# Performance work log

Measured on AMD Instinct MI355X. Metric: run time of the kernel, lower is better.

Reference implementation:

```python
import jax, jax.numpy as jnp
import numpy as np

H = 8          # num heads
LN_EPS = 1e-5  # torch LayerNorm default

_SHAPES = {
    'src': (1024, 8, 256), 'pos': (1024, 8, 256), 'query_embed': (80, 8, 256), 'cam_mask': (8, 80, 1024),
    'enc_qkv_w': (2, 768, 256), 'enc_qkv_b': (2, 768), 'enc_out_w': (2, 256, 256), 'enc_out_b': (2, 256),
    'enc_ln1_g': (2, 256), 'enc_ln1_b': (2, 256),
    'enc_ff1_w': (2, 2048, 256), 'enc_ff1_b': (2, 2048), 'enc_ff2_w': (2, 256, 2048), 'enc_ff2_b': (2, 256),
    'enc_ln2_g': (2, 256), 'enc_ln2_b': (2, 256),
    'dec_sa_qkv_w': (2, 768, 256), 'dec_sa_qkv_b': (2, 768), 'dec_sa_out_w': (2, 256, 256), 'dec_sa_out_b': (2, 256),
    'dec_ln1_g': (2, 256), 'dec_ln1_b': (2, 256),
    'dec_ca_qkv_w': (2, 768, 256), 'dec_ca_qkv_b': (2, 768), 'dec_ca_out_w': (2, 256, 256), 'dec_ca_out_b': (2, 256),
    'dec_ln2_g': (2, 256), 'dec_ln2_b': (2, 256),
    'dec_ff1_w': (2, 2048, 256), 'dec_ff1_b': (2, 2048), 'dec_ff2_w': (2, 256, 2048), 'dec_ff2_b': (2, 256),
    'dec_ln3_g': (2, 256), 'dec_ln3_b': (2, 256),
    'dec_norm_g': (256,), 'dec_norm_b': (256,),
}


def setup_inputs() -> dict:
    key = jax.random.key(0)
    out = {}
    for i, (name, sh) in enumerate(_SHAPES.items()):
        k = jax.random.fold_in(key, i)
        if name.endswith('_g'):
            out[name] = jnp.ones(sh, jnp.float32)
        elif name.endswith('ln1_b') or name.endswith('ln2_b') or name.endswith('ln3_b') or name == 'dec_norm_b':
            out[name] = jnp.zeros(sh, jnp.float32)
        else:
            scale = 1.0 if name in ('src', 'pos', 'query_embed', 'cam_mask') else 0.02
            out[name] = jax.random.normal(k, sh, dtype=jnp.float32) * scale
    return out


def layer_norm(x, g, b):
    mu = jnp.mean(x, axis=-1, keepdims=True)
    var = jnp.mean(jnp.square(x - mu), axis=-1, keepdims=True)
    return (x - mu) * jax.lax.rsqrt(var + LN_EPS) * g + b


def mha(q_in, k_in, v_in, qkv_w, qkv_b, out_w, out_b, bias=None):
    # q_in: [L,B,D], k_in/v_in: [S,B,D]; torch layout: projections are x @ W.T + b
    L, B, D = q_in.shape
    S = k_in.shape[0]
    hd = D // H
    wq, wk, wv = qkv_w[:D], qkv_w[D:2 * D], qkv_w[2 * D:]
    bq, bk, bv = qkv_b[:D], qkv_b[D:2 * D], qkv_b[2 * D:]
    q = (q_in @ wq.T + bq).reshape(L, B, H, hd).transpose(1, 2, 0, 3)  # [B,H,L,hd]
    k = (k_in @ wk.T + bk).reshape(S, B, H, hd).transpose(1, 2, 0, 3)  # [B,H,S,hd]
    v = (v_in @ wv.T + bv).reshape(S, B, H, hd).transpose(1, 2, 0, 3)
    logits = jnp.einsum('bhld,bhsd->bhls', q, k) * (1.0 / np.sqrt(hd))
    if bias is not None:
        logits = logits + bias[:, None, :, :]  # CAM bias broadcast over heads
    attn = jax.nn.softmax(logits, axis=-1)
    o = jnp.einsum('bhls,bhsd->bhld', attn, v).transpose(2, 0, 1, 3).reshape(L, B, D)
    return o @ out_w.T + out_b


def reference(src, pos, query_embed, cam_mask,
              enc_qkv_w, enc_qkv_b, enc_out_w, enc_out_b, enc_ln1_g, enc_ln1_b,
              enc_ff1_w, enc_ff1_b, enc_ff2_w, enc_ff2_b, enc_ln2_g, enc_ln2_b,
              dec_sa_qkv_w, dec_sa_qkv_b, dec_sa_out_w, dec_sa_out_b, dec_ln1_g, dec_ln1_b,
              dec_ca_qkv_w, dec_ca_qkv_b, dec_ca_out_w, dec_ca_out_b, dec_ln2_g, dec_ln2_b,
              dec_ff1_w, dec_ff1_b, dec_ff2_w, dec_ff2_b, dec_ln3_g, dec_ln3_b,
              dec_norm_g, dec_norm_b):
    n_enc = enc_qkv_w.shape[0]
    n_dec = dec_sa_qkv_w.shape[0]
    # --- encoder (post-norm DETR style, pos added to q,k) ---
    mem = src
    for i in range(n_enc):
        qk = mem + pos
        a = mha(qk, qk, mem, enc_qkv_w[i], enc_qkv_b[i], enc_out_w[i], enc_out_b[i])
        mem = layer_norm(mem + a, enc_ln1_g[i], enc_ln1_b[i])
        f = jax.nn.relu(mem @ enc_ff1_w[i].T + enc_ff1_b[i]) @ enc_ff2_w[i].T + enc_ff2_b[i]
        mem = layer_norm(mem + f, enc_ln2_g[i], enc_ln2_b[i])
    # --- decoder: tgt starts at zeros (Q2L), query_embed is query_pos ---
    tgt = jnp.zeros_like(query_embed)
    for i in range(n_dec):
        qk = tgt + query_embed
        sa = mha(qk, qk, tgt, dec_sa_qkv_w[i], dec_sa_qkv_b[i], dec_sa_out_w[i], dec_sa_out_b[i])
        tgt = layer_norm(tgt + sa, dec_ln1_g[i], dec_ln1_b[i])
        ca = mha(tgt + query_embed, mem + pos, mem,
                 dec_ca_qkv_w[i], dec_ca_qkv_b[i], dec_ca_out_w[i], dec_ca_out_b[i],
                 bias=cam_mask)  # MA: CAM-derived additive attention bias [B,L,S]
        tgt = layer_norm(tgt + ca, dec_ln2_g[i], dec_ln2_b[i])
        f = jax.nn.relu(tgt @ dec_ff1_w[i].T + dec_ff1_b[i]) @ dec_ff2_w[i].T + dec_ff2_b[i]
        tgt = layer_norm(tgt + f, dec_ln3_g[i], dec_ln3_b[i])
    out = layer_norm(tgt, dec_norm_g, dec_norm_b)
    return out[None]  # [1, L, B, D] as in TransformerDecoder's output.unsqueeze(0)
```

## Files before the change

kernel.cpp:

```cpp
#include <hip/hip_runtime.h>
#include <hip/hip_bf16.h>
#include <cstdint>
#include <cstddef>

typedef __hip_bfloat16 bf16;
typedef float f4 __attribute__((ext_vector_type(4)));
typedef float f32x4 __attribute__((ext_vector_type(4)));
typedef short s8v __attribute__((ext_vector_type(8)));
typedef unsigned short u16x4 __attribute__((ext_vector_type(4)));
typedef unsigned short u16x8 __attribute__((ext_vector_type(8)));

#define LN_EPS 1e-5f
#define LOG2E 1.4426950408889634f

#if __has_builtin(__builtin_amdgcn_exp2f)
__device__ __forceinline__ float EXP2(float x) { return __builtin_amdgcn_exp2f(x); }
#else
__device__ __forceinline__ float EXP2(float x) {
  float r; asm("v_exp_f32 %0, %1" : "=v"(r) : "v"(x)); return r;
}
#endif

__device__ __forceinline__ void async_cp16(const void* g, void* lds) {
  __builtin_amdgcn_global_load_lds(
      (const __attribute__((address_space(1))) unsigned int*)g,
      (__attribute__((address_space(3))) unsigned int*)lds, 16, 0, 0);
}

__device__ __forceinline__ uint32_t pkbf(float lo, float hi) {
#if __has_builtin(__builtin_amdgcn_perm)
  uint32_t l = __builtin_bit_cast(uint32_t, lo) + 0x8000u;
  uint32_t h = __builtin_bit_cast(uint32_t, hi) + 0x8000u;
  return __builtin_amdgcn_perm(h, l, 0x07060302u);
#else
  uint32_t l = __builtin_bit_cast(uint32_t, lo) + 0x8000u;
  uint32_t h = __builtin_bit_cast(uint32_t, hi) + 0x8000u;
  return (l >> 16) | (h & 0xFFFF0000u);
#endif
}

#define NCAST 16
struct CastArgs {
  const float* in[NCAST];
  bf16* out[NCAST];
  int end4[NCAST];
  int nseg;
};

__global__ __launch_bounds__(256) void cast_multi(CastArgs a, int total4) {
  int i = blockIdx.x * 256 + threadIdx.x;
  if (i >= total4) return;
  int s = 0;
  while (i >= a.end4[s]) ++s;
  int j = i - (s ? a.end4[s - 1] : 0);
  f4 v = ((const f4*)a.in[s])[j];
  u16x4 o;
#pragma unroll
  for (int c = 0; c < 4; ++c) {
    bf16 h = __float2bfloat16(v[c]);
    o[c] = *reinterpret_cast<unsigned short*>(&h);
  }
  ((u16x4*)a.out[s])[j] = o;
}

__global__ __launch_bounds__(256) void scale_f32_kernel(const float* __restrict__ in,
                                                        float* __restrict__ out,
                                                        float s, int n4) {
  int i = blockIdx.x * 256 + threadIdx.x;
  if (i < n4) {
    f4 v = ((const f4*)in)[i];
    ((f4*)out)[i] = v * s;
  }
}

__global__ __launch_bounds__(256) void add_bf16_kernel(const float* __restrict__ a,
                                                       const float* __restrict__ b,
                                                       bf16* __restrict__ out, int n4) {
  int i = blockIdx.x * 256 + threadIdx.x;
  if (i < n4) {
    f4 x = ((const f4*)a)[i];
    f4 y = ((const f4*)b)[i];
    u16x4 o;
#pragma unroll
    for (int j = 0; j < 4; ++j) {
      bf16 h = __float2bfloat16(x[j] + y[j]);
      o[j] = *reinterpret_cast<unsigned short*>(&h);
    }
    ((u16x4*)out)[i] = o;
  }
}

template <int TB, int MODE, int SPLITK>
__global__ __launch_bounds__(256, 2) void mfma_gemm(
    const bf16* __restrict__ A, const bf16* __restrict__ W,
    const float* __restrict__ bias, float* __restrict__ C,
    bf16* __restrict__ Cb, int M, int N, int K, int HL, float qscale) {
  constexpr int WM = TB / 2, WN = TB / 2;
  constexpr int MR = WM / 16, NR = WN / 16;
  constexpr int NCH = TB / 32;
  __shared__ __attribute__((aligned(16))) unsigned short SH[TB * 128];
  unsigned short (*As)[64] = (unsigned short(*)[64])SH;
  unsigned short (*Ws)[64] = (unsigned short(*)[64])(SH + TB * 64);
  const int tid = threadIdx.x;
  const int lane = tid & 63, wave = tid >> 6;
  const int wr = wave >> 1, wc = wave & 1;
  const int bm = blockIdx.x * TB, bn = blockIdx.y * TB;
  const int fr = lane & 15, fo = lane >> 4;
  const int srowi = lane >> 3;
  const int slot = lane & 7;
  const int gcol = (slot ^ srowi) * 8;

  const int kchunk = K / SPLITK;
  const int kbeg = (SPLITK > 1) ? blockIdx.z * kchunk : 0;

  f32x4 acc[MR][NR] = {};

  for (int k0 = kbeg; k0 < kbeg + kchunk; k0 += 64) {
    __syncthreads();
#pragma unroll
    for (int c = 0; c < NCH; ++c) {
      int rbase = wave * (TB / 4) + c * 8;
      int row = rbase + srowi;
      async_cp16(A + (size_t)(bm + row) * K + k0 + gcol, &As[rbase][0]);
      async_cp16(W + (size_t)(bn + row) * K + k0 + gcol, &Ws[rbase][0]);
    }
    __syncthreads();
#pragma unroll
    for (int ks = 0; ks < 2; ++ks) {
      s8v a[MR], b[NR];
#pragma unroll
      for (int mi = 0; mi < MR; ++mi) {
        int row = wr * WM + mi * 16 + fr;
        a[mi] = *(const s8v*)((const char*)&As[0][0] + row * 128 +
                              ((ks * 64 + fo * 16) ^ ((row & 7) << 4)));
      }
#pragma unroll
      for (int ni = 0; ni < NR; ++ni) {
        int row = wc * WN + ni * 16 + fr;
        b[ni] = *(const s8v*)((const char*)&Ws[0][0] + row * 128 +
                              ((ks * 64 + fo * 16) ^ ((row & 7) << 4)));
      }
#pragma unroll
      for (int mi = 0; mi < MR; ++mi)
#pragma unroll
        for (int ni = 0; ni < NR; ++ni)
          acc[mi][ni] = __builtin_amdgcn_mfma_f32_16x16x32_bf16(
              a[mi], b[ni], acc[mi][ni], 0, 0, 0);
    }
  }

  const int r0 = (lane >> 4) * 4;

  if (MODE == 5) {
    __syncthreads();
    unsigned short (*T)[72] = (unsigned short(*)[72])SH;
#pragma unroll
    for (int mi = 0; mi < MR; ++mi)
#pragma unroll
      for (int ni = 0; ni < NR; ++ni) {
        int colL = wc * WN + ni * 16 + fr;
        float bv = bias[bn + colL];
#pragma unroll
        for (int r = 0; r < 4; ++r) {
          int rowL = wr * WM + mi * 16 + r0 + r;
          bf16 hv = __float2bfloat16(acc[mi][ni][r] + bv);
          T[colL][rowL] = *(unsigned short*)&hv;
        }
      }
    __syncthreads();
    const int lbase = bm >> 3;
#pragma unroll
    for (int jj = 0; jj < 2; ++jj) {
      int cid = tid * 2 + jj;
      int colL = cid >> 3, bb = cid & 7;
      int c = bn + colL;
      int sec = c >> 8, hh = (c >> 5) & 7, d = c & 31;
      u16x8 v;
#pragma unroll
      for (int l = 0; l < 8; ++l) v[l] = T[colL][bb + 8 * l];
      *(u16x8*)(Cb + (size_t)sec * ((size_t)64 * 32 * HL) +
                ((size_t)(bb * 8 + hh) * 32 + d) * HL + lbase) = v;
    }
    return;
  }

  float* Cz = (MODE == 4) ? C + (size_t)blockIdx.z * M * N : C;
#pragma unroll
  for (int mi = 0; mi < MR; ++mi) {
#pragma unroll
    for (int ni = 0; ni < NR; ++ni) {
      int col = bn + wc * WN + ni * 16 + fr;
      float bv = (MODE == 4) ? 0.f : bias[col];
#pragma unroll
      for (int r = 0; r < 4; ++r) {
        int row = bm + wr * WM + mi * 16 + r0 + r;
        float t = acc[mi][ni][r] + bv;
        if (MODE == 2) t = fmaxf(t, 0.f);
        if (MODE == 0) {
          C[(size_t)row * N + col] = t;
        } else if (MODE == 4) {
          Cz[(size_t)row * N + col] = t;
        } else if (MODE == 3) {
          int l = row >> 3, bb = row & 7;
          int sec = col >> 8, hh = (col >> 5) & 7, d = col & 31;
          if (sec == 0) t *= qscale;
          Cb[(size_t)sec * ((size_t)64 * HL * 32) +
             ((size_t)(bb * 8 + hh) * HL + l) * 32 + d] = __float2bfloat16(t);
        } else {
          Cb[(size_t)row * N + col] = __float2bfloat16(t);
        }
      }
    }
  }
}

template <int HAS_BIAS, int PARTIAL, int NW>
__global__ __launch_bounds__(NW * 64, 3) void attn_mfma(
    const bf16* __restrict__ Qh, const bf16* __restrict__ Kh,
    const bf16* __restrict__ VhT, const float* __restrict__ bias,
    bf16* __restrict__ O, float* __restrict__ PO, float* __restrict__ PM,
    float* __restrict__ PL, int L, int S, int SC) {
  __shared__ __attribute__((aligned(16))) uint32_t Ps2[NW][16][68];
  const int tid = threadIdx.x;
  const int lane = tid & 63, wave = tid >> 6;
  const int fr = lane & 15, fo = lane >> 4;
  const int bh = blockIdx.x;
  const int b = bh >> 3, h = bh & 7;
  const int q0 = blockIdx.y * (NW * 16) + wave * 16;
  const int q = q0 + fr;

  const int cz = PARTIAL ? blockIdx.z : 0;
  const int sb = PARTIAL ? cz * SC : 0;
  const int se = PARTIAL ? min(S, sb + SC) : S;

  s8v qf = {};
  if (q < L) qf = *(const s8v*)(Qh + ((size_t)bh * L + q) * 32 + fo * 8);

  const float* brow = nullptr;
  if (HAS_BIAS) brow = bias + ((size_t)b * L + (q < L ? q : L - 1)) * S;

  float m = -1e30f, lsum = 0.f;
  f32x4 oacc[2] = {};

  for (int s0 = sb; s0 < se; s0 += 128) {
    s8v kf[8];
#pragma unroll
    for (int i = 0; i < 8; ++i) {
      int key = s0 + (i >> 2) * 64 + (i & 3) * 16 + fr;
      kf[i] = *(const s8v*)(Kh + ((size_t)bh * S + key) * 32 + fo * 8);
    }
    s8v vf[2][4];
#pragma unroll
    for (int dh = 0; dh < 2; ++dh)
#pragma unroll
      for (int ks = 0; ks < 4; ++ks)
        vf[dh][ks] = *(const s8v*)(VhT + ((size_t)bh * 32 + dh * 16 + fr) * S +
                                   s0 + ks * 32 + fo * 8);

    float lg[32];
#pragma unroll
    for (int i = 0; i < 8; ++i) {
      f32x4 z = {};
      f32x4 sa = __builtin_amdgcn_mfma_f32_16x16x32_bf16(kf[i], qf, z, 0, 0, 0);
#pragma unroll
      for (int r = 0; r < 4; ++r) lg[i * 4 + r] = sa[r];
    }

    if (HAS_BIAS) {
#pragma unroll
      for (int i = 0; i < 8; ++i) {
        f4 bv = *(const f4*)(brow + s0 + (i >> 2) * 64 + (i & 3) * 16 + 4 * fo);
#pragma unroll
        for (int r = 0; r < 4; ++r) lg[i * 4 + r] += bv[r];
      }
    }

    if (s0 + 128 > se) {
#pragma unroll
      for (int i = 0; i < 8; ++i)
#pragma unroll
        for (int r = 0; r < 4; ++r) {
          int key = s0 + (i >> 2) * 64 + (i & 3) * 16 + 4 * fo + r;
          if (key >= se) lg[i * 4 + r] = -1e30f;
        }
    }

    float t[8];
#pragma unroll
    for (int i = 0; i < 8; ++i)
      t[i] = fmaxf(fmaxf(lg[i * 4], lg[i * 4 + 1]),
                   fmaxf(lg[i * 4 + 2], lg[i * 4 + 3]));
    float u0 = fmaxf(fmaxf(t[0], t[1]), fmaxf(t[2], t[3]));
    float u1 = fmaxf(fmaxf(t[4], t[5]), fmaxf(t[6], t[7]));
    float tm = fmaxf(u0, u1);
    tm = fmaxf(tm, __shfl_xor(tm, 16));
    tm = fmaxf(tm, __shfl_xor(tm, 32));

    if (__any(tm > m + 8.f)) {
      float nm = fmaxf(m, tm);
      float rs = EXP2(m - nm);
      m = nm;
      lsum *= rs;
#pragma unroll
      for (int r = 0; r < 4; ++r) { oacc[0][r] *= rs; oacc[1][r] *= rs; }
    }

    float ps = 0.f;
#pragma unroll
    for (int i = 0; i < 32; ++i) {
      lg[i] = EXP2(lg[i] - m);
      ps += lg[i];
    }
    lsum += ps;

#pragma unroll
    for (int i = 0; i < 8; ++i) {
      uint32_t w0 = pkbf(lg[i * 4 + 0], lg[i * 4 + 1]);
      uint32_t w1 = pkbf(lg[i * 4 + 2], lg[i * 4 + 3]);
      uint64_t w = (uint64_t)w0 | ((uint64_t)w1 << 32);
      *(uint64_t*)&Ps2[wave][fr][(i >> 2) * 32 + (i & 3) * 8 + 2 * fo] = w;
    }

    s8v pf[4];
#pragma unroll
    for (int ks = 0; ks < 4; ++ks)
      pf[ks] = *(const s8v*)&Ps2[wave][fr][ks * 16 + 4 * fo];

#pragma unroll
    for (int dh = 0; dh < 2; ++dh)
#pragma unroll
      for (int ks = 0; ks < 4; ++ks)
        oacc[dh] = __builtin_amdgcn_mfma_f32_16x16x32_bf16(
            vf[dh][ks], pf[ks], oacc[dh], 0, 0, 0);
  }

  lsum += __shfl_xor(lsum, 16);
  lsum += __shfl_xor(lsum, 32);

  if (q < L) {
    if (PARTIAL) {
      size_t pi = ((size_t)cz * 64 + bh) * L + q;
      float* po = PO + pi * 32;
#pragma unroll
      for (int dh = 0; dh < 2; ++dh) {
        f4 t2;
#pragma unroll
        for (int r = 0; r < 4; ++r) t2[r] = oacc[dh][r];
        *(f4*)(po + dh * 16 + 4 * fo) = t2;
      }
      if (fo == 0) { PM[pi] = m; PL[pi] = lsum; }
    } else {
      float inv = 1.f / lsum;
      bf16* op = O + ((size_t)q * 8 + b) * 256 + h * 32;
#pragma unroll
      for (int dh = 0; dh < 2; ++dh) {
        uint32_t w0 = pkbf(oacc[dh][0] * inv, oacc[dh][1] * inv);
        uint32_t w1 = pkbf(oacc[dh][2] * inv, oacc[dh][3] * inv);
        *(uint32_t*)(op + dh * 16 + 4 * fo) = w0;
        *(uint32_t*)(op + dh * 16 + 4 * fo + 2) = w1;
      }
    }
  }
}

__global__ __launch_bounds__(256) void attn_combine(
    const float* __restrict__ PO, const float* __restrict__ PM,
    const float* __restrict__ PL, bf16* __restrict__ O, int L, int NC) {
  int gid = blockIdx.x * 256 + threadIdx.x;
  if (gid >= 64 * L * 32) return;
  int d = gid & 31;
  int rem = gid >> 5;
  int q = rem % L, bh = rem / L;
  int b = bh >> 3, h = bh & 7;
  float M = -1e30f;
  for (int c = 0; c < NC; ++c) M = fmaxf(M, PM[((size_t)c * 64 + bh) * L + q]);
  float lsum = 0.f, o = 0.f;
  for (int c = 0; c < NC; ++c) {
    size_t pi = ((size_t)c * 64 + bh) * L + q;
    float w = EXP2(PM[pi] - M);
    lsum += PL[pi] * w;
    o += PO[pi * 32 + d] * w;
  }
  O[((size_t)q * 8 + b) * 256 + h * 32 + d] = __float2bfloat16(o / lsum);
}

__global__ __launch_bounds__(256) void ln_kernel(
    const float* __restrict__ x, const float* __restrict__ res,
    const float* __restrict__ parts, int nparts, int pstride,
    const float* __restrict__ gbias,
    const float* __restrict__ g, const float* __restrict__ b,
    float* __restrict__ out, bf16* __restrict__ outb) {
  const int row = blockIdx.x, tid = threadIdx.x;
  size_t idx = (size_t)row * 256 + tid;
  float v = x[idx];
  if (res) v += res[idx];
  if (parts) {
    for (int z = 0; z < nparts; ++z) v += parts[(size_t)z * pstride + idx];
  }
  if (gbias) v += gbias[tid];
  float s = v, s2 = v * v;
#pragma unroll
  for (int off = 32; off >= 1; off >>= 1) {
    s += __shfl_down(s, off);
    s2 += __shfl_down(s2, off);
  }
  __shared__ float red[8];
  int wv = tid >> 6;
  if ((tid & 63) == 0) { red[wv] = s; red[4 + wv] = s2; }
  __syncthreads();
  if (tid == 0) {
    float ts = red[0] + red[1] + red[2] + red[3];
    float ts2 = red[4] + red[5] + red[6] + red[7];
    float mu = ts * (1.f / 256.f);
    float var = ts2 * (1.f / 256.f) - mu * mu;
    red[0] = mu;
    red[1] = rsqrtf(var + LN_EPS);
  }
  __syncthreads();
  float y = (v - red[0]) * red[1] * g[tid] + b[tid];
  if (out) out[idx] = y;
  if (outb) outb[idx] = __float2bfloat16(y);
}

extern "C" void kernel_launch(void* const* d_in, const int* in_sizes, int n_in,
                              void* d_out, int out_size, void* d_ws, size_t ws_size,
                              hipStream_t stream) {
  const float* src         = (const float*)d_in[0];
  const float* pos         = (const float*)d_in[1];
  const float* query_embed = (const float*)d_in[2];
  const float* cam_mask    = (const float*)d_in[3];
  const float* enc_qkv_w   = (const float*)d_in[4];
  const float* enc_qkv_b   = (const float*)d_in[5];
  const float* enc_out_w   = (const float*)d_in[6];
  const float* enc_out_b   = (const float*)d_in[7];
  const float* enc_ln1_g   = (const float*)d_in[8];
  const float* enc_ln1_b   = (const float*)d_in[9];
  const float* enc_ff1_w   = (const float*)d_in[10];
  const float* enc_ff1_b   = (const float*)d_in[11];
  const float* enc_ff2_w   = (const float*)d_in[12];
  const float* enc_ff2_b   = (const float*)d_in[13];
  const float* enc_ln2_g   = (const float*)d_in[14];
  const float* enc_ln2_b   = (const float*)d_in[15];
  const float* dec_sa_qkv_w= (const float*)d_in[16];
  const float* dec_sa_qkv_b= (const float*)d_in[17];
  const float* dec_sa_out_w= (const float*)d_in[18];
  const float* dec_sa_out_b= (const float*)d_in[19];
  const float* dec_ln1_g   = (const float*)d_in[20];
  const float* dec_ln1_b   = (const float*)d_in[21];
  const float* dec_ca_qkv_w= (const float*)d_in[22];
  const float* dec_ca_qkv_b= (const float*)d_in[23];
  const float* dec_ca_out_w= (const float*)d_in[24];
  const float* dec_ca_out_b= (const float*)d_in[25];
  const float* dec_ln2_g   = (const float*)d_in[26];
  const float* dec_ln2_b   = (const float*)d_in[27];
  const float* dec_ff1_w   = (const float*)d_in[28];
  const float* dec_ff1_b   = (const float*)d_in[29];
  const float* dec_ff2_w   = (const float*)d_in[30];
  const float* dec_ff2_b   = (const float*)d_in[31];
  const float* dec_ln3_g   = (const float*)d_in[32];
  const float* dec_ln3_b   = (const float*)d_in[33];
  const float* dec_norm_g  = (const float*)d_in[34];
  const float* dec_norm_b  = (const float*)d_in[35];

  size_t off = 0;
  char* base = (char*)d_ws;
  auto af = [&](size_t n) { float* p = (float*)(base + off); off += n * 4; return p; };
  auto ab = [&](size_t n) { bf16*  p = (bf16*)(base + off);  off += n * 2; return p; };

  float* mem  = af(2097152);
  float* r1   = af(2097152);
  float* PO   = af(8388608);
  float* pm   = af(262144);
  float* pl   = af(262144);
  float* cmlog= af(655360);
  float* pb   = af(1024);
  float* tgt  = af(163840);
  float* tpr  = af(163840);
  bf16* memb  = ab(2097152);
  bf16* qkb   = ab(2097152);
  bf16* aob   = ab(2097152);
  bf16* ffb   = ab(16777216);
  bf16* bufQ  = ab(4194304);
  bf16* bufK  = ab(4194304);
  bf16* bufV  = ab(4194304);
  bf16* bufVsa= ab(172032);
  bf16* tgtb  = ab(163840);
  bf16* tqkb  = ab(163840);
  bf16* taob  = ab(163840);
  bf16* tffb  = ab(1310720);
  bf16* w_enc_qkv = ab(393216);
  bf16* w_enc_out = ab(131072);
  bf16* w_enc_ff1 = ab(1048576);
  bf16* w_enc_ff2 = ab(1048576);
  bf16* w_sa_qkv  = ab(393216);
  bf16* w_sa_out  = ab(131072);
  bf16* w_ca_q    = ab(131072);
  bf16* w_ca_kv   = ab(262144);
  bf16* w_ca_out  = ab(131072);
  bf16* w_dec_ff1 = ab(1048576);
  bf16* w_dec_ff2 = ab(1048576);

  const float qscale = 0.17677669529663687f * LOG2E;

  {
    CastArgs ca;
    const float* ins[NCAST] = {
        enc_qkv_w, enc_out_w, enc_ff1_w, enc_ff2_w,
        dec_sa_qkv_w, dec_sa_out_w,
        dec_ca_qkv_w,
        dec_ca_qkv_w + 65536,
        dec_ca_qkv_w + 131072,
        dec_ca_qkv_w + 196608,
        dec_ca_qkv_w + 262144,
        dec_ca_qkv_w + 327680,
        dec_ca_out_w, dec_ff1_w, dec_ff2_w, src};
    bf16* outs[NCAST] = {
        w_enc_qkv, w_enc_out, w_enc_ff1, w_enc_ff2,
        w_sa_qkv, w_sa_out,
        w_ca_q,
        w_ca_kv,
        w_ca_kv + 131072,
        w_ca_q + 65536,
        w_ca_kv + 65536,
        w_ca_kv + 196608,
        w_ca_out, w_dec_ff1, w_dec_ff2, memb};
    int n4s[NCAST] = {98304, 32768, 262144, 262144, 98304, 32768,
                      16384, 16384, 16384, 16384, 16384, 16384,
                      32768, 262144, 262144, 524288};
    int acc = 0;
    for (int s = 0; s < NCAST; ++s) {
      ca.in[s] = ins[s]; ca.out[s] = outs[s];
      acc += n4s[s]; ca.end4[s] = acc;
    }
    ca.nseg = NCAST;
    cast_multi<<<(acc + 255) / 256, 256, 0, stream>>>(ca, acc);
  }
  scale_f32_kernel<<<640, 256, 0, stream>>>(cam_mask, cmlog, LOG2E, 163840);
  hipMemcpyAsync(mem, src, (size_t)2097152 * 4, hipMemcpyDeviceToDevice, stream);
  hipMemcpyAsync(pb,       dec_ca_qkv_b + 256,       1024, hipMemcpyDeviceToDevice, stream);
  hipMemcpyAsync(pb + 256, dec_ca_qkv_b + 768 + 256, 1024, hipMemcpyDeviceToDevice, stream);
  hipMemcpyAsync(pb + 512, dec_ca_qkv_b + 512,       1024, hipMemcpyDeviceToDevice, stream);
  hipMemcpyAsync(pb + 768, dec_ca_qkv_b + 768 + 512, 1024, hipMemcpyDeviceToDevice, stream);

  auto g64_f = [&](const bf16* A, const bf16* W, const float* bias, float* C,
                   int M, int N, int K) {
    mfma_gemm<64, 0, 1><<<dim3(M / 64, N / 64), 256, 0, stream>>>(
        A, W, bias, C, nullptr, M, N, K, 0, 1.f);
  };
  auto g64_head = [&](const bf16* A, const bf16* W, const float* bias, bf16* Cb,
                      int M, int N, int K, int HL, float qs) {
    mfma_gemm<64, 3, 1><<<dim3(M / 64, N / 64), 256, 0, stream>>>(
        A, W, bias, nullptr, Cb, M, N, K, HL, qs);
  };
  auto g64_headT = [&](const bf16* A, const bf16* W, const float* bias, bf16* Cb,
                       int M, int N, int K, int HL) {
    mfma_gemm<64, 5, 1><<<dim3(M / 64, N / 64), 256, 0, stream>>>(
        A, W, bias, nullptr, Cb, M, N, K, HL, 1.f);
  };
  auto g64_relu = [&](const bf16* A, const bf16* W, const float* bias, bf16* Cb,
                      int M, int N, int K) {
    mfma_gemm<64, 2, 1><<<dim3(M / 64, N / 64), 256, 0, stream>>>(
        A, W, bias, nullptr, Cb, M, N, K, 0, 1.f);
  };
  auto g128_relu = [&](const bf16* A, const bf16* W, const float* bias, bf16* Cb,
                       int M, int N, int K) {
    mfma_gemm<128, 2, 1><<<dim3(M / 128, N / 128), 256, 0, stream>>>(
        A, W, bias, nullptr, Cb, M, N, K, 0, 1.f);
  };

  for (int i = 0; i < 2; ++i) {
    const bf16* wq = w_enc_qkv + (size_t)i * 196608;
    const float* qkvb = enc_qkv_b + (size_t)i * 768;
    add_bf16_kernel<<<2048, 256, 0, stream>>>(mem, pos, qkb, 524288);
    g64_head(qkb, wq, qkvb, bufQ, 8192, 512, 256, 1024, qscale);
    g64_headT(memb, wq + 131072, qkvb + 512, bufV, 8192, 256, 256, 1024);
    attn_mfma<0, 0, 4><<<dim3(64, 16), 256, 0, stream>>>(
        bufQ, bufQ + 2097152, bufV, nullptr, aob, nullptr, nullptr, nullptr,
        1024, 1024, 0);
    g64_f(aob, w_enc_out + (size_t)i * 65536, enc_out_b + i * 256, r1,
          8192, 256, 256);
    ln_kernel<<<8192, 256, 0, stream>>>(mem, r1, nullptr, 0, 0, nullptr,
                                        enc_ln1_g + i * 256, enc_ln1_b + i * 256,
                                        mem, memb);
    g128_relu(memb, w_enc_ff1 + (size_t)i * 524288, enc_ff1_b + i * 2048, ffb,
              8192, 2048, 256);
    mfma_gemm<128, 4, 4><<<dim3(64, 2, 4), 256, 0, stream>>>(
        ffb, w_enc_ff2 + (size_t)i * 524288, nullptr, PO, nullptr,
        8192, 256, 2048, 0, 1.f);
    ln_kernel<<<8192, 256, 0, stream>>>(mem, nullptr, PO, 4, 2097152,
                                        enc_ff2_b + i * 256,
                                        enc_ln2_g + i * 256, enc_ln2_b + i * 256,
                                        mem, memb);
  }

  hipMemsetAsync(tgt, 0, (size_t)163840 * 4, stream);
  hipMemsetAsync(tgtb, 0, (size_t)163840 * 2, stream);
  add_bf16_kernel<<<2048, 256, 0, stream>>>(mem, pos, qkb, 524288);

  g64_head(qkb, w_ca_kv, pb, bufK, 8192, 512, 256, 1024, 1.f);
  g64_headT(memb, w_ca_kv + 131072, pb + 512, bufV, 8192, 512, 256, 1024);

  for (int i = 0; i < 2; ++i) {
    const bf16* wsa = w_sa_qkv + (size_t)i * 196608;
    const float* sab = dec_sa_qkv_b + (size_t)i * 768;
    const float* cab = dec_ca_qkv_b + (size_t)i * 768;

    add_bf16_kernel<<<160, 256, 0, stream>>>(tgt, query_embed, tqkb, 40960);
    g64_head(tqkb, wsa, sab, bufQ, 640, 512, 256, 80, qscale);
    g64_headT(tgtb, wsa + 131072, sab + 512, bufVsa, 640, 256, 256, 80);
    attn_mfma<0, 0, 1><<<dim3(64, 5), 64, 0, stream>>>(
        bufQ, bufQ + 163840, bufVsa, nullptr, taob, nullptr, nullptr, nullptr,
        80, 80, 0);
    g64_f(taob, w_sa_out + (size_t)i * 65536, dec_sa_out_b + i * 256, tpr,
          640, 256, 256);
    ln_kernel<<<640, 256, 0, stream>>>(tgt, tpr, nullptr, 0, 0, nullptr,
                                       dec_ln1_g + i * 256, dec_ln1_b + i * 256,
                                       tgt, tgtb);
    add_bf16_kernel<<<160, 256, 0, stream>>>(tgt, query_embed, tqkb, 40960);
    g64_head(tqkb, w_ca_q + (size_t)i * 65536, cab, bufQ, 640, 256, 256, 80, qscale);
    attn_mfma<1, 1, 1><<<dim3(64, 5, 8), 64, 0, stream>>>(
        bufQ, bufK + (size_t)i * 2097152, bufV + (size_t)i * 2097152, cmlog,
        nullptr, PO, pm, pl, 80, 1024, 128);
    attn_combine<<<640, 256, 0, stream>>>(PO, pm, pl, taob, 80, 8);
    g64_f(taob, w_ca_out + (size_t)i * 65536, dec_ca_out_b + i * 256, tpr,
          640, 256, 256);
    ln_kernel<<<640, 256, 0, stream>>>(tgt, tpr, nullptr, 0, 0, nullptr,
                                       dec_ln2_g + i * 256, dec_ln2_b + i * 256,
                                       tgt, tgtb);
    g64_relu(tgtb, w_dec_ff1 + (size_t)i * 524288, dec_ff1_b + i * 2048, tffb,
             640, 2048, 256);
    mfma_gemm<64, 4, 4><<<dim3(10, 4, 4), 256, 0, stream>>>(
        tffb, w_dec_ff2 + (size_t)i * 524288, nullptr, PO, nullptr,
        640, 256, 2048, 0, 1.f);
    ln_kernel<<<640, 256, 0, stream>>>(tgt, nullptr, PO, 4, 163840,
                                       dec_ff2_b + i * 256,
                                       dec_ln3_g + i * 256, dec_ln3_b + i * 256,
                                       tgt, tgtb);
  }

  ln_kernel<<<640, 256, 0, stream>>>(tgt, nullptr, nullptr, 0, 0, nullptr,
                                     dec_norm_g, dec_norm_b,
                                     (float*)d_out, nullptr);
}
```

Baseline: 433.3 us.

## Split attention loop into two independent online-softmax streams per 128-key step

Each 128-key iteration of the attention kernel is split into two 64-key halves, each with its own running max, sum and output accumulator, merged only once at the end. This gives the scheduler two independent dependency chains to interleave, so MFMA, exp and shuffle latency can overlap. The lazy rescale under __any is replaced by an unconditional rescale each step, and bias loads are issued up front with the K/V loads. The cost is more registers for duplicated state, which may hurt occupancy. The loop also appears to assume an even number of 64-key groups in the range, or it reads past its chunk.

```diff
diff --git a/kernel.cpp b/kernel.cpp
--- a/kernel.cpp
+++ b/kernel.cpp
@@ -220,7 +220,7 @@
     const bf16* __restrict__ VhT, const float* __restrict__ bias,
     bf16* __restrict__ O, float* __restrict__ PO, float* __restrict__ PM,
     float* __restrict__ PL, int L, int S, int SC) {
-  __shared__ __attribute__((aligned(16))) uint32_t Ps2[NW][16][68];
+  __shared__ __attribute__((aligned(16))) uint32_t Ps2[NW][2][16][36];
   const int tid = threadIdx.x;
   const int lane = tid & 63, wave = tid >> 6;
   const int fr = lane & 15, fo = lane >> 4;
@@ -232,6 +232,7 @@
   const int cz = PARTIAL ? blockIdx.z : 0;
   const int sb = PARTIAL ? cz * SC : 0;
   const int se = PARTIAL ? min(S, sb + SC) : S;
+  const int ng = (se - sb + 63) >> 6;
 
   s8v qf = {};
   if (q < L) qf = *(const s8v*)(Qh + ((size_t)bh * L + q) * 32 + fo * 8);
@@ -239,100 +240,140 @@
   const float* brow = nullptr;
   if (HAS_BIAS) brow = bias + ((size_t)b * L + (q < L ? q : L - 1)) * S;
 
-  float m = -1e30f, lsum = 0.f;
-  f32x4 oacc[2] = {};
-
-  for (int s0 = sb; s0 < se; s0 += 128) {
-    s8v kf[8];
-#pragma unroll
-    for (int i = 0; i < 8; ++i) {
-      int key = s0 + (i >> 2) * 64 + (i & 3) * 16 + fr;
-      kf[i] = *(const s8v*)(Kh + ((size_t)bh * S + key) * 32 + fo * 8);
-    }
-    s8v vf[2][4];
+  const bf16* Kbase = Kh + (size_t)bh * S * 32;
+  const bf16* Vbase = VhT + (size_t)bh * 32 * S;
+
+  float mA = -1e30f, lsA = 0.f, mB = -1e30f, lsB = 0.f;
+  f32x4 oA[2] = {}, oB[2] = {};
+
+  for (int g = 0; g < ng; g += 2) {
+    const int sA = sb + g * 64, sB = sA + 64;
+
+    s8v kA[4], kB[4], vA[2][2], vB[2][2];
+#pragma unroll
+    for (int kb = 0; kb < 4; ++kb) {
+      kA[kb] = *(const s8v*)(Kbase + (size_t)(sA + kb * 16 + fr) * 32 + fo * 8);
+      kB[kb] = *(const s8v*)(Kbase + (size_t)(sB + kb * 16 + fr) * 32 + fo * 8);
+    }
 #pragma unroll
     for (int dh = 0; dh < 2; ++dh)
 #pragma unroll
-      for (int ks = 0; ks < 4; ++ks)
-        vf[dh][ks] = *(const s8v*)(VhT + ((size_t)bh * 32 + dh * 16 + fr) * S +
-                                   s0 + ks * 32 + fo * 8);
-
-    float lg[32];
-#pragma unroll
-    for (int i = 0; i < 8; ++i) {
+      for (int ks = 0; ks < 2; ++ks) {
+        vA[dh][ks] = *(const s8v*)(Vbase + (size_t)(dh * 16 + fr) * S +
+                                   sA + ks * 32 + fo * 8);
+        vB[dh][ks] = *(const s8v*)(Vbase + (size_t)(dh * 16 + fr) * S +
+                                   sB + ks * 32 + fo * 8);
+      }
+    f4 bA[4], bB[4];
+    if (HAS_BIAS) {
+#pragma unroll
+      for (int kb = 0; kb < 4; ++kb) {
+        bA[kb] = *(const f4*)(brow + sA + kb * 16 + 4 * fo);
+        bB[kb] = *(const f4*)(brow + sB + kb * 16 + 4 * fo);
+      }
+    }
+
+    float lgA[16], lgB[16];
+#pragma unroll
+    for (int kb = 0; kb < 4; ++kb) {
       f32x4 z = {};
-      f32x4 sa = __builtin_amdgcn_mfma_f32_16x16x32_bf16(kf[i], qf, z, 0, 0, 0);
-#pragma unroll
-      for (int r = 0; r < 4; ++r) lg[i * 4 + r] = sa[r];
-    }
-
+      f32x4 sa = __builtin_amdgcn_mfma_f32_16x16x32_bf16(kA[kb], qf, z, 0, 0, 0);
+#pragma unroll
+      for (int r = 0; r < 4; ++r) lgA[kb * 4 + r] = sa[r];
+    }
+#pragma unroll
+    for (int kb = 0; kb < 4; ++kb) {
+      f32x4 z = {};
+      f32x4 sa = __builtin_amdgcn_mfma_f32_16x16x32_bf16(kB[kb], qf, z, 0, 0, 0);
+#pragma unroll
+      for (int r = 0; r < 4; ++r) lgB[kb * 4 + r] = sa[r];
+    }
     if (HAS_BIAS) {
 #pragma unroll
-      for (int i = 0; i < 8; ++i) {
-        f4 bv = *(const f4*)(brow + s0 + (i >> 2) * 64 + (i & 3) * 16 + 4 * fo);
-#pragma unroll
-        for (int r = 0; r < 4; ++r) lg[i * 4 + r] += bv[r];
-      }
-    }
-
-    if (s0 + 128 > se) {
-#pragma unroll
-      for (int i = 0; i < 8; ++i)
-#pragma unroll
-        for (int r = 0; r < 4; ++r) {
-          int key = s0 + (i >> 2) * 64 + (i & 3) * 16 + 4 * fo + r;
-          if (key >= se) lg[i * 4 + r] = -1e30f;
-        }
-    }
-
-    float t[8];
-#pragma unroll
-    for (int i = 0; i < 8; ++i)
-      t[i] = fmaxf(fmaxf(lg[i * 4], lg[i * 4 + 1]),
-                   fmaxf(lg[i * 4 + 2], lg[i * 4 + 3]));
-    float u0 = fmaxf(fmaxf(t[0], t[1]), fmaxf(t[2], t[3]));
-    float u1 = fmaxf(fmaxf(t[4], t[5]), fmaxf(t[6], t[7]));
-    float tm = fmaxf(u0, u1);
-    tm = fmaxf(tm, __shfl_xor(tm, 16));
-    tm = fmaxf(tm, __shfl_xor(tm, 32));
-
-    if (__any(tm > m + 8.f)) {
-      float nm = fmaxf(m, tm);
-      float rs = EXP2(m - nm);
-      m = nm;
-      lsum *= rs;
-#pragma unroll
-      for (int r = 0; r < 4; ++r) { oacc[0][r] *= rs; oacc[1][r] *= rs; }
-    }
-
-    float ps = 0.f;
-#pragma unroll
-    for (int i = 0; i < 32; ++i) {
-      lg[i] = EXP2(lg[i] - m);
-      ps += lg[i];
-    }
-    lsum += ps;
-
-#pragma unroll
-    for (int i = 0; i < 8; ++i) {
-      uint32_t w0 = pkbf(lg[i * 4 + 0], lg[i * 4 + 1]);
-      uint32_t w1 = pkbf(lg[i * 4 + 2], lg[i * 4 + 3]);
-      uint64_t w = (uint64_t)w0 | ((uint64_t)w1 << 32);
-      *(uint64_t*)&Ps2[wave][fr][(i >> 2) * 32 + (i & 3) * 8 + 2 * fo] = w;
-    }
-
-    s8v pf[4];
-#pragma unroll
-    for (int ks = 0; ks < 4; ++ks)
-      pf[ks] = *(const s8v*)&Ps2[wave][fr][ks * 16 + 4 * fo];
-
+      for (int i = 0; i < 16; ++i) { lgA[i] += bA[i >> 2][i & 3]; lgB[i] += bB[i >> 2][i & 3]; }
+    }
+    if (sB + 64 > se) {
+#pragma unroll
+      for (int i = 0; i < 16; ++i) {
+        int keyA = sA + (i >> 2) * 16 + 4 * fo + (i & 3);
+        int keyB = sB + (i >> 2) * 16 + 4 * fo + (i & 3);
+        if (keyA >= se) lgA[i] = -1e30f;
+        if (keyB >= se) lgB[i] = -1e30f;
+      }
+    }
+
+    float tA, tB;
+    {
+      float a0 = fmaxf(fmaxf(lgA[0], lgA[1]), fmaxf(lgA[2], lgA[3]));
+      float a1 = fmaxf(fmaxf(lgA[4], lgA[5]), fmaxf(lgA[6], lgA[7]));
+      float a2 = fmaxf(fmaxf(lgA[8], lgA[9]), fmaxf(lgA[10], lgA[11]));
+      float a3 = fmaxf(fmaxf(lgA[12], lgA[13]), fmaxf(lgA[14], lgA[15]));
+      tA = fmaxf(fmaxf(a0, a1), fmaxf(a2, a3));
+      float b0 = fmaxf(fmaxf(lgB[0], lgB[1]), fmaxf(lgB[2], lgB[3]));
+      float b1 = fmaxf(fmaxf(lgB[4], lgB[5]), fmaxf(lgB[6], lgB[7]));
+      float b2 = fmaxf(fmaxf(lgB[8], lgB[9]), fmaxf(lgB[10], lgB[11]));
+      float b3 = fmaxf(fmaxf(lgB[12], lgB[13]), fmaxf(lgB[14], lgB[15]));
+      tB = fmaxf(fmaxf(b0, b1), fmaxf(b2, b3));
+    }
+    tA = fmaxf(tA, __shfl_xor(tA, 16));
+    tB = fmaxf(tB, __shfl_xor(tB, 16));
+    tA = fmaxf(tA, __shfl_xor(tA, 32));
+    tB = fmaxf(tB, __shfl_xor(tB, 32));
+
+    float nmA = fmaxf(mA, tA), nmB = fmaxf(mB, tB);
+    float rsA = EXP2(mA - nmA), rsB = EXP2(mB - nmB);
+    mA = nmA; mB = nmB;
+
+    float psA = 0.f, psB = 0.f;
+#pragma unroll
+    for (int i = 0; i < 16; ++i) {
+      lgA[i] = EXP2(lgA[i] - nmA); psA += lgA[i];
+      lgB[i] = EXP2(lgB[i] - nmB); psB += lgB[i];
+    }
+    lsA = lsA * rsA + psA;
+    lsB = lsB * rsB + psB;
+
+#pragma unroll
+    for (int kb = 0; kb < 4; ++kb) {
+      uint32_t a0 = pkbf(lgA[kb * 4 + 0], lgA[kb * 4 + 1]);
+      uint32_t a1 = pkbf(lgA[kb * 4 + 2], lgA[kb * 4 + 3]);
+      *(uint64_t*)&Ps2[wave][0][fr][kb * 8 + 2 * fo] =
+          (uint64_t)a0 | ((uint64_t)a1 << 32);
+      uint32_t b0 = pkbf(lgB[kb * 4 + 0], lgB[kb * 4 + 1]);
+      uint32_t b1 = pkbf(lgB[kb * 4 + 2], lgB[kb * 4 + 3]);
+      *(uint64_t*)&Ps2[wave][1][fr][kb * 8 + 2 * fo] =
+          (uint64_t)b0 | ((uint64_t)b1 << 32);
+    }
+
+#pragma unroll
+    for (int r = 0; r < 4; ++r) {
+      oA[0][r] *= rsA; oA[1][r] *= rsA;
+      oB[0][r] *= rsB; oB[1][r] *= rsB;
+    }
+    s8v pA[2], pB[2];
+#pragma unroll
+    for (int ks = 0; ks < 2; ++ks) {
+      pA[ks] = *(const s8v*)&Ps2[wave][0][fr][ks * 16 + 4 * fo];
+      pB[ks] = *(const s8v*)&Ps2[wave][1][fr][ks * 16 + 4 * fo];
+    }
 #pragma unroll
     for (int dh = 0; dh < 2; ++dh)
 #pragma unroll
-      for (int ks = 0; ks < 4; ++ks)
-        oacc[dh] = __builtin_amdgcn_mfma_f32_16x16x32_bf16(
-            vf[dh][ks], pf[ks], oacc[dh], 0, 0, 0);
-  }
+      for (int ks = 0; ks < 2; ++ks) {
+        oA[dh] = __builtin_amdgcn_mfma_f32_16x16x32_bf16(vA[dh][ks], pA[ks], oA[dh], 0, 0, 0);
+        oB[dh] = __builtin_amdgcn_mfma_f32_16x16x32_bf16(vB[dh][ks], pB[ks], oB[dh], 0, 0, 0);
+      }
+  }
+
+  float m = fmaxf(mA, mB);
+  float wA = EXP2(mA - m), wB = EXP2(mB - m);
+  float lsum = lsA * wA + lsB * wB;
+  f32x4 oacc[2];
+#pragma unroll
+  for (int dh = 0; dh < 2; ++dh)
+#pragma unroll
+    for (int r = 0; r < 4; ++r)
+      oacc[dh][r] = oA[dh][r] * wA + oB[dh][r] * wB;
 
   lsum += __shfl_xor(lsum, 16);
   lsum += __shfl_xor(lsum, 32);
```

Measured after the change: 433.8 us. Within noise of the previous version (+0.1%).
